# Kernel tuning notes

Hardware: AMD Instinct MI355X
Metric: run time of the kernel (lower is better)

The kernel has to match this reference:

```python
import jax, jax.numpy as jnp
import numpy as np

N_LOW, N_HIGH = 5000, 50000
E_LH, E_HH = 200000, 400000


def _gatv2(xs, xd, src, dst, Wl, bl, Wr, br, att, bias, n_dst):
    """PyG GATv2Conv with aggr='mean', concat heads. att: [H, C]."""
    H, C = att.shape
    hl = (xs @ Wl + bl).reshape(-1, H, C)   # source transform (messages)
    hr = (xd @ Wr + br).reshape(-1, H, C)   # target transform
    z = jax.nn.leaky_relu(hl[src] + hr[dst], 0.2)        # [E, H, C]
    logit = jnp.einsum('ehc,hc->eh', z, att)             # [E, H]
    m = jax.lax.stop_gradient(jax.ops.segment_max(logit, dst, num_segments=n_dst))
    ex = jnp.exp(logit - m[dst])
    s = jax.ops.segment_sum(ex, dst, num_segments=n_dst)
    alpha = ex / (s[dst] + 1e-16)                        # edge softmax per dst, per head
    msg = hl[src] * alpha[..., None]                     # [E, H, C]
    out = jax.ops.segment_sum(msg, dst, num_segments=n_dst)
    cnt = jax.ops.segment_sum(jnp.ones(dst.shape, xs.dtype), dst, num_segments=n_dst)
    out = out / jnp.maximum(cnt, 1.0)[:, None, None]     # aggr='mean'
    return out.reshape(n_dst, H * C) + bias


def _bn(x, g, b):
    mu = x.mean(0)
    var = x.var(0)
    return (x - mu) * jax.lax.rsqrt(var + 1e-5) * g + b


def setup_inputs() -> dict:
    key = jax.random.key(0)
    it = iter(jax.random.split(key, 64))
    def nk():
        return next(it)
    def glorot(shape):
        s = np.sqrt(2.0 / (shape[0] + shape[-1])).astype(np.float32)
        return jax.random.normal(nk(), shape, jnp.float32) * s
    inp = {}
    inp['xl'] = jax.random.normal(nk(), (N_LOW, 125), jnp.float32)
    inp['xh'] = jax.random.normal(nk(), (N_HIGH, 1), jnp.float32)
    inp['zstd'] = jax.random.normal(nk(), (N_HIGH, 1), jnp.float32)
    inp['si_lh'] = jax.random.randint(nk(), (E_LH,), 0, N_LOW, jnp.int32)
    inp['di_lh'] = jax.random.randint(nk(), (E_LH,), 0, N_HIGH, jnp.int32)
    inp['si_hh'] = jax.random.randint(nk(), (E_HH,), 0, N_HIGH, jnp.int32)
    inp['di_hh'] = jax.random.randint(nk(), (E_HH,), 0, N_HIGH, jnp.int32)
    def gat(pfx, fs, fd, H, C):
        inp[pfx + '_Wl'] = glorot((fs, H * C)); inp[pfx + '_bl'] = jnp.zeros((H * C,), jnp.float32)
        inp[pfx + '_Wr'] = glorot((fd, H * C)); inp[pfx + '_br'] = jnp.zeros((H * C,), jnp.float32)
        inp[pfx + '_att'] = glorot((H, C)); inp[pfx + '_b'] = jnp.zeros((H * C,), jnp.float32)
    gat('d', 125, 1, 1, 256)
    gat('p1', 257, 257, 4, 64)
    gat('p2', 256, 256, 4, 64)
    gat('p3', 256, 256, 1, 64)
    for pfx, dim in [('bn0', 257), ('bn1', 256), ('bn2', 256), ('bn3', 64)]:
        inp[pfx + '_g'] = jnp.ones((dim,), jnp.float32)
        inp[pfx + '_b'] = jnp.zeros((dim,), jnp.float32)
    inp['pr_W1'] = glorot((64, 64)); inp['pr_b1'] = jnp.zeros((64,), jnp.float32)
    inp['pr_W2'] = glorot((64, 1)); inp['pr_b2'] = jnp.zeros((1,), jnp.float32)
    return inp


def reference(xl, xh, zstd, si_lh, di_lh, si_hh, di_hh,
              d_Wl, d_bl, d_Wr, d_br, d_att, d_b,
              p1_Wl, p1_bl, p1_Wr, p1_br, p1_att, p1_b,
              p2_Wl, p2_bl, p2_Wr, p2_br, p2_att, p2_b,
              p3_Wl, p3_bl, p3_Wr, p3_br, p3_att, p3_b,
              bn0_g, bn0_b, bn1_g, bn1_b, bn2_g, bn2_b, bn3_g, bn3_b,
              pr_W1, pr_b1, pr_W2, pr_b2):
    n_high = xh.shape[0]
    # downscaler: bipartite GATv2 (low -> high), heads=1, no self loops
    enc = _gatv2(xl, xh, si_lh, di_lh, d_Wl, d_bl, d_Wr, d_br, d_att, d_b, n_high)
    x = jnp.concatenate([zstd, enc], axis=-1)            # [N_HIGH, 257]
    # high-within-high edges with self loops (add_self_loops=True)
    loop = jnp.arange(n_high, dtype=si_hh.dtype)
    src = jnp.concatenate([si_hh, loop])
    dst = jnp.concatenate([di_hh, loop])
    x = _bn(x, bn0_g, bn0_b)
    x = _gatv2(x, x, src, dst, p1_Wl, p1_bl, p1_Wr, p1_br, p1_att, p1_b, n_high)
    x = jax.nn.relu(_bn(x, bn1_g, bn1_b))
    x = _gatv2(x, x, src, dst, p2_Wl, p2_bl, p2_Wr, p2_br, p2_att, p2_b, n_high)
    x = jax.nn.relu(_bn(x, bn2_g, bn2_b))
    x = _gatv2(x, x, src, dst, p3_Wl, p3_bl, p3_Wr, p3_br, p3_att, p3_b, n_high)
    x = jax.nn.relu(_bn(x, bn3_g, bn3_b))
    # predictor MLP
    y = jax.nn.relu(x @ pr_W1 + pr_b1) @ pr_W2 + pr_b2   # [N_HIGH, 1]
    return y
```

## Files before the change

kernel.cpp:

```cpp
#include <hip/hip_runtime.h>
#include <math.h>

#define DEV __device__ __forceinline__

static const int N_LOW = 5000, N_HIGH = 50000, E_LH = 200000, E_HH = 400000;
static const int E2 = E_HH + N_HIGH;
static const int ETOT = E_LH + E2;
static const int RBLK = 2048;

typedef __attribute__((ext_vector_type(8))) short bf16x8;
typedef __attribute__((ext_vector_type(4))) float f32x4;
typedef __attribute__((ext_vector_type(8))) unsigned short u16x8;
typedef unsigned short u16;

DEV short f2bf(float v) {
    unsigned u = __float_as_uint(v);
    u += 0x7FFFu + ((u >> 16) & 1u);
    return (short)(u >> 16);
}
DEV float bf2f(u16 u) { return __uint_as_float(((unsigned)u) << 16); }

template <int VPL> struct RawTT { using T = u16; };
template <> struct RawTT<4> { using T = ushort4; };

template <bool RELU, bool BF16OUT>
DEV void gemm_body(const bf16x8* __restrict__ Af, const bf16x8* __restrict__ Bf,
                   const float* __restrict__ bias, float* __restrict__ C,
                   int M, int N, int nkt) {
    const int l = threadIdx.x & 63;
    const int w = threadIdx.x >> 6;
    const int nt0 = blockIdx.x * 4;
    const int mt0 = blockIdx.y * 8 + w * 2;
    f32x4 acc[2][4];
#pragma unroll
    for (int i = 0; i < 2; i++)
#pragma unroll
        for (int j = 0; j < 4; j++) acc[i][j] = (f32x4){0.f, 0.f, 0.f, 0.f};
    const bf16x8* a0p = Af + (size_t)mt0 * nkt * 64 + l;
    const bf16x8* a1p = a0p + (size_t)nkt * 64;
    const bf16x8* bp = Bf + (size_t)nt0 * nkt * 64 + l;
    for (int kt = 0; kt < nkt; kt++) {
        bf16x8 a0 = a0p[kt * 64];
        bf16x8 a1 = a1p[kt * 64];
        bf16x8 b0 = bp[kt * 64];
        bf16x8 b1 = bp[(size_t)(nkt + kt) * 64];
        bf16x8 b2 = bp[(size_t)(2 * nkt + kt) * 64];
        bf16x8 b3 = bp[(size_t)(3 * nkt + kt) * 64];
        acc[0][0] = __builtin_amdgcn_mfma_f32_16x16x32_bf16(a0, b0, acc[0][0], 0, 0, 0);
        acc[0][1] = __builtin_amdgcn_mfma_f32_16x16x32_bf16(a0, b1, acc[0][1], 0, 0, 0);
        acc[0][2] = __builtin_amdgcn_mfma_f32_16x16x32_bf16(a0, b2, acc[0][2], 0, 0, 0);
        acc[0][3] = __builtin_amdgcn_mfma_f32_16x16x32_bf16(a0, b3, acc[0][3], 0, 0, 0);
        acc[1][0] = __builtin_amdgcn_mfma_f32_16x16x32_bf16(a1, b0, acc[1][0], 0, 0, 0);
        acc[1][1] = __builtin_amdgcn_mfma_f32_16x16x32_bf16(a1, b1, acc[1][1], 0, 0, 0);
        acc[1][2] = __builtin_amdgcn_mfma_f32_16x16x32_bf16(a1, b2, acc[1][2], 0, 0, 0);
        acc[1][3] = __builtin_amdgcn_mfma_f32_16x16x32_bf16(a1, b3, acc[1][3], 0, 0, 0);
    }
    const int colb = nt0 * 16 + (l & 15);
    const int rsub = (l >> 4) * 4;
#pragma unroll
    for (int mi = 0; mi < 2; mi++) {
        int rowb = (mt0 + mi) * 16 + rsub;
#pragma unroll
        for (int r = 0; r < 4; r++) {
            int row = rowb + r;
            if (row >= M) continue;
#pragma unroll
            for (int n = 0; n < 4; n++) {
                int col = colb + n * 16;
                float v = acc[mi][n][r] + bias[col];
                if (RELU) v = fmaxf(v, 0.f);
                if (BF16OUT)
                    ((u16*)C)[(size_t)row * N + col] = (u16)f2bf(v);
                else
                    C[(size_t)row * N + col] = v;
            }
        }
    }
}

template <bool RELU, bool BF16OUT>
__global__ __launch_bounds__(256) void gemm_mfma(
    const bf16x8* __restrict__ Af, const bf16x8* __restrict__ Bf,
    const float* __restrict__ bias, float* __restrict__ C,
    int M, int N, int nkt) {
    gemm_body<RELU, BF16OUT>(Af, Bf, bias, C, M, N, nkt);
}

__global__ __launch_bounds__(256) void gemm_mfma2(
    const bf16x8* __restrict__ Af,
    const bf16x8* __restrict__ Bf0, const bf16x8* __restrict__ Bf1,
    const float* __restrict__ bias0, const float* __restrict__ bias1,
    float* __restrict__ C0, float* __restrict__ C1,
    int M, int N, int nkt) {
    if (blockIdx.z == 0)
        gemm_body<false, true>(Af, Bf0, bias0, C0, M, N, nkt);
    else
        gemm_body<false, true>(Af, Bf1, bias1, C1, M, N, nkt);
}

template <bool RELU>
__global__ __launch_bounds__(256) void bn_frag(
    const u16* __restrict__ x, int Nrows, int F, int STR, int SS,
    const float* __restrict__ sums,
    const float* __restrict__ g, const float* __restrict__ b,
    bf16x8* __restrict__ Af, int nmt, int nkt) {
    int total = nmt * nkt * 64;
    for (int idx = blockIdx.x * blockDim.x + threadIdx.x; idx < total;
         idx += gridDim.x * blockDim.x) {
        int mt = idx / (nkt * 64);
        int rem = idx - mt * (nkt * 64);
        int kt = rem >> 6, l = rem & 63;
        int row = mt * 16 + (l & 15);
        int colb = kt * 32 + (l >> 4) * 8;
        bf16x8 o;
#pragma unroll
        for (int j = 0; j < 8; j++) {
            int col = colb + j;
            float v = 0.f;
            if (row < Nrows && col < F) {
                float mu = sums[col] / Nrows;
                float var = sums[SS + col] / Nrows - mu * mu;
                float istd = rsqrtf(fmaxf(var, 0.f) + 1e-5f);
                v = (bf2f(x[(size_t)row * STR + col]) - mu) * istd * g[col] + b[col];
                if (RELU) v = fmaxf(v, 0.f);
            }
            o[j] = f2bf(v);
        }
        Af[idx] = o;
    }
}

__global__ __launch_bounds__(256) void cast_frag(
    const float* __restrict__ x, int Nrows, int F,
    bf16x8* __restrict__ Af, int nmt, int nkt) {
    int total = nmt * nkt * 64;
    for (int idx = blockIdx.x * blockDim.x + threadIdx.x; idx < total;
         idx += gridDim.x * blockDim.x) {
        int mt = idx / (nkt * 64);
        int rem = idx - mt * (nkt * 64);
        int kt = rem >> 6, l = rem & 63;
        int row = mt * 16 + (l & 15);
        int colb = kt * 32 + (l >> 4) * 8;
        bf16x8 o;
#pragma unroll
        for (int j = 0; j < 8; j++) {
            int col = colb + j;
            o[j] = (row < Nrows && col < F) ? f2bf(x[(size_t)row * F + col]) : (short)0;
        }
        Af[idx] = o;
    }
}

struct WtJobs {
    const float* W[8];
    bf16x8* out[8];
    int K[8], Nn[8], nnt[8], nkt[8];
};
__global__ __launch_bounds__(256) void wt_frag_all(WtJobs jobs) {
    const int job = blockIdx.y;
    const float* W = jobs.W[job];
    bf16x8* Bf = jobs.out[job];
    const int K = jobs.K[job], N = jobs.Nn[job];
    const int nkt = jobs.nkt[job];
    int total = jobs.nnt[job] * nkt * 64;
    for (int idx = blockIdx.x * blockDim.x + threadIdx.x; idx < total;
         idx += gridDim.x * blockDim.x) {
        int nt = idx / (nkt * 64);
        int rem = idx - nt * (nkt * 64);
        int kt = rem >> 6, l = rem & 63;
        int col = nt * 16 + (l & 15);
        int kb = kt * 32 + (l >> 4) * 8;
        bf16x8 o;
#pragma unroll
        for (int j = 0; j < 8; j++) {
            int k = kb + j;
            o[j] = (k < K && col < N) ? f2bf(W[(size_t)k * N + col]) : (short)0;
        }
        Bf[idx] = o;
    }
}

__global__ __launch_bounds__(256) void hist_all(
    const int* __restrict__ di_lh, const int* __restrict__ di_hh,
    int* __restrict__ cnt) {
    for (int i = blockIdx.x * blockDim.x + threadIdx.x; i < ETOT;
         i += gridDim.x * blockDim.x) {
        if (i < E_LH) {
            atomicAdd(&cnt[di_lh[i]], 1);
        } else {
            int j = i - E_LH;
            int d = (j < E_HH) ? di_hh[j] : (j - E_HH);
            atomicAdd(&cnt[N_HIGH + d], 1);
        }
    }
}

__global__ __launch_bounds__(256) void scan_partial(
    const int* __restrict__ cnt, int* __restrict__ off,
    int* __restrict__ bsum, int n) {
    __shared__ int s[256];
    const int t = threadIdx.x;
    const int base = blockIdx.x * 1024 + t * 4;
    int v0 = (base < n) ? cnt[base] : 0;
    int v1 = (base + 1 < n) ? cnt[base + 1] : 0;
    int v2 = (base + 2 < n) ? cnt[base + 2] : 0;
    int v3 = (base + 3 < n) ? cnt[base + 3] : 0;
    int tsum = v0 + v1 + v2 + v3;
    s[t] = tsum;
    __syncthreads();
    for (int step = 1; step < 256; step <<= 1) {
        int q = (t >= step) ? s[t - step] : 0;
        __syncthreads();
        s[t] += q;
        __syncthreads();
    }
    int excl = s[t] - tsum;
    if (base < n) off[base] = excl;
    if (base + 1 < n) off[base + 1] = excl + v0;
    if (base + 2 < n) off[base + 2] = excl + v0 + v1;
    if (base + 3 < n) off[base + 3] = excl + v0 + v1 + v2;
    if (t == 255) bsum[blockIdx.x] = s[255];
}

__global__ __launch_bounds__(256) void scan_bsums(
    int* __restrict__ bsum, int nb, int* __restrict__ off, int n) {
    __shared__ int s[256];
    const int t = threadIdx.x;
    int v = (t < nb) ? bsum[t] : 0;
    s[t] = v;
    __syncthreads();
    for (int step = 1; step < 256; step <<= 1) {
        int q = (t >= step) ? s[t - step] : 0;
        __syncthreads();
        s[t] += q;
        __syncthreads();
    }
    if (t < nb) bsum[t] = s[t] - v;
    if (t == 255) off[n] = s[255];
}

__global__ __launch_bounds__(256) void scan_add(
    int* __restrict__ off, const int* __restrict__ bsum, int n) {
    int b = blockIdx.x;
    int add = bsum[b];
    int base = b * 1024;
    int end = base + 1024 < n ? base + 1024 : n;
    for (int i = base + threadIdx.x; i < end; i += 256) off[i] += add;
}

__global__ __launch_bounds__(256) void scatter_all(
    const int* __restrict__ si_lh, const int* __restrict__ di_lh,
    const int* __restrict__ si_hh, const int* __restrict__ di_hh,
    int* __restrict__ cur, int* __restrict__ csr) {
    for (int i = blockIdx.x * blockDim.x + threadIdx.x; i < ETOT;
         i += gridDim.x * blockDim.x) {
        int d, s, bucket;
        if (i < E_LH) {
            d = di_lh[i]; s = si_lh[i]; bucket = d;
        } else {
            int j = i - E_LH;
            if (j < E_HH) { d = di_hh[j]; s = si_hh[j]; }
            else { d = s = j - E_HH; }
            bucket = N_HIGH + d;
        }
        int p = atomicAdd(&cur[bucket], 1);
        csr[p] = s;
    }
}

template <int H, int C, bool HR_ONFLY>
__global__ __launch_bounds__(256) void gat_gather(
    const u16* __restrict__ hl, const u16* __restrict__ hr,
    const float* __restrict__ xh, const float* __restrict__ Wr,
    const float* __restrict__ br,
    const int* __restrict__ rowptr, const int* __restrict__ csr_src,
    const float* __restrict__ att, const float* __restrict__ bias,
    u16* __restrict__ out, int outStride, int outOfs, int Ndst,
    const float* __restrict__ col0) {
    constexpr int HC = H * C;
    constexpr int VPL = HC / 64;
    constexpr int LPH = C / VPL;
    using RawT = typename RawTT<VPL>::T;
    int w = blockIdx.x * (blockDim.x >> 6) + (threadIdx.x >> 6);
    if (w >= Ndst) return;
    const int l = threadIdx.x & 63;

    float hrv[VPL], attv[VPL];
    if constexpr (HR_ONFLY) {
        static_assert(!HR_ONFLY || VPL == 4, "onfly assumes VPL==4");
        float xv = xh[w];
        float4 wr = *reinterpret_cast<const float4*>(Wr + l * 4);
        float4 bb = *reinterpret_cast<const float4*>(br + l * 4);
        hrv[0] = fmaf(xv, wr.x, bb.x); hrv[1] = fmaf(xv, wr.y, bb.y);
        hrv[2] = fmaf(xv, wr.z, bb.z); hrv[3] = fmaf(xv, wr.w, bb.w);
        float4 u = *reinterpret_cast<const float4*>(att + l * 4);
        attv[0] = u.x; attv[1] = u.y; attv[2] = u.z; attv[3] = u.w;
    } else if constexpr (VPL == 4) {
        ushort4 t = *(reinterpret_cast<const ushort4*>(hr + (size_t)w * HC) + l);
        hrv[0] = bf2f(t.x); hrv[1] = bf2f(t.y); hrv[2] = bf2f(t.z); hrv[3] = bf2f(t.w);
        float4 u = *reinterpret_cast<const float4*>(att + l * 4);
        attv[0] = u.x; attv[1] = u.y; attv[2] = u.z; attv[3] = u.w;
    } else {
#pragma unroll
        for (int j = 0; j < VPL; j++) {
            hrv[j] = bf2f(hr[(size_t)w * HC + l * VPL + j]);
            attv[j] = att[l * VPL + j];
        }
    }

    const int e0 = rowptr[w], e1 = rowptr[w + 1];
    float m = -3.4e38f, s = 0.f;
    float acc[VPL] = {};

    auto ldraw = [&](int sv) -> RawT {
        if constexpr (VPL == 4)
            return *(reinterpret_cast<const ushort4*>(hl + (size_t)sv * HC) + l);
        else
            return hl[(size_t)sv * HC + l];
    };
    auto proc = [&](RawT t) {
        float hlv[VPL];
        if constexpr (VPL == 4) {
            hlv[0] = bf2f(t.x); hlv[1] = bf2f(t.y);
            hlv[2] = bf2f(t.z); hlv[3] = bf2f(t.w);
        } else {
            hlv[0] = bf2f(t);
        }
        float v = 0.f;
#pragma unroll
        for (int j = 0; j < VPL; j++) {
            float z = hlv[j] + hrv[j];
            v = fmaf(fmaxf(z, 0.2f * z), attv[j], v);
        }
#pragma unroll
        for (int t2 = 1; t2 < LPH; t2 <<= 1) v += __shfl_xor(v, t2, 64);
        float d = v - m;
        bool up = d > 0.f;
        float ef = __expf(-fabsf(d));
        float sc = up ? ef : 1.f;
        float p  = up ? 1.f : ef;
        m = up ? v : m;
        s = fmaf(s, sc, p);
#pragma unroll
        for (int j = 0; j < VPL; j++) acc[j] = fmaf(acc[j], sc, p * hlv[j]);
    };

    int e = e0;
    for (; e + 3 < e1; e += 4) {
        int sv0 = csr_src[e];
        int sv1 = csr_src[e + 1];
        int sv2 = csr_src[e + 2];
        int sv3 = csr_src[e + 3];
        RawT t0 = ldraw(sv0);
        RawT t1 = ldraw(sv1);
        RawT t2 = ldraw(sv2);
        RawT t3 = ldraw(sv3);
        proc(t0); proc(t1); proc(t2); proc(t3);
    }
    for (; e < e1; e++) {
        RawT t = ldraw(csr_src[e]);
        proc(t);
    }

    float inv = 1.f / (s + 1e-16f);
    float dnorm = inv / fmaxf((float)(e1 - e0), 1.f);
    if constexpr (VPL == 4) {
        if (((outOfs | outStride) & 3) == 0) {
            ushort4 o;
            o.x = (u16)f2bf(acc[0] * dnorm + bias[l * 4 + 0]);
            o.y = (u16)f2bf(acc[1] * dnorm + bias[l * 4 + 1]);
            o.z = (u16)f2bf(acc[2] * dnorm + bias[l * 4 + 2]);
            o.w = (u16)f2bf(acc[3] * dnorm + bias[l * 4 + 3]);
            *(reinterpret_cast<ushort4*>(out + (size_t)w * outStride + outOfs) + l) = o;
        } else {
#pragma unroll
            for (int j = 0; j < 4; j++)
                out[(size_t)w * outStride + outOfs + l * 4 + j] =
                    (u16)f2bf(acc[j] * dnorm + bias[l * 4 + j]);
        }
    } else {
#pragma unroll
        for (int j = 0; j < VPL; j++)
            out[(size_t)w * outStride + outOfs + l * VPL + j] =
                (u16)f2bf(acc[j] * dnorm + bias[l * VPL + j]);
    }
    if (col0 && l == 0) out[(size_t)w * outStride] = (u16)f2bf(col0[w]);
}

template <int NC, int RPB>
__global__ __launch_bounds__(256) void bn_partial3(
    const u16* __restrict__ x, int Nrows, float* __restrict__ partials) {
    constexpr int STR = NC * 8;
    constexpr int NSTAT = 2 * NC * 8;
    const int t = threadIdx.x;
    const int b = blockIdx.x;
    __shared__ float l1[NC * RPB * 8];
    __shared__ float l2[NC * RPB * 8];
    float s1[8] = {}, s2[8] = {};
    if (t < NC * RPB) {
        const int rg = t / NC, cg = t - (t / NC) * NC;
        for (int r = b * RPB + rg; r < Nrows; r += RBLK * RPB) {
            u16x8 p = *reinterpret_cast<const u16x8*>(x + (size_t)r * STR + cg * 8);
#pragma unroll
            for (int j = 0; j < 8; j++) {
                float v = bf2f(p[j]);
                s1[j] += v; s2[j] += v * v;
            }
        }
#pragma unroll
        for (int j = 0; j < 8; j++) {
            l1[t * 8 + j] = s1[j];
            l2[t * 8 + j] = s2[j];
        }
    }
    __syncthreads();
    if (t < NC) {
        float a[8] = {}, c[8] = {};
#pragma unroll
        for (int rg = 0; rg < RPB; rg++)
#pragma unroll
            for (int j = 0; j < 8; j++) {
                a[j] += l1[(rg * NC + t) * 8 + j];
                c[j] += l2[(rg * NC + t) * 8 + j];
            }
#pragma unroll
        for (int j = 0; j < 8; j++) {
            partials[(size_t)b * NSTAT + t * 8 + j] = a[j];
            partials[(size_t)b * NSTAT + NC * 8 + t * 8 + j] = c[j];
        }
    }
}

__global__ __launch_bounds__(256) void bn_reduce2(
    const float* __restrict__ partials, int nstat, float* __restrict__ bsum) {
    const int sl = threadIdx.x & 63, ch = threadIdx.x >> 6;
    const int s = blockIdx.x * 64 + sl;
    const int b0 = blockIdx.y * (RBLK / 32);
    float v = 0.f;
    if (s < nstat) {
        for (int b = b0 + ch; b < b0 + RBLK / 32; b += 4)
            v += partials[(size_t)b * nstat + s];
    }
    __shared__ float l[256];
    l[threadIdx.x] = v;
    __syncthreads();
    if (ch == 0 && s < nstat)
        atomicAdd(&bsum[s], l[sl] + l[sl + 64] + l[sl + 128] + l[sl + 192]);
}

__global__ __launch_bounds__(256) void dot_w2(const float* __restrict__ hid,
                                              const float* __restrict__ W2,
                                              const float* __restrict__ b2,
                                              float* __restrict__ y, int N) {
    int w = blockIdx.x * (blockDim.x >> 6) + (threadIdx.x >> 6);
    int l = threadIdx.x & 63;
    if (w >= N) return;
    float v = hid[(size_t)w * 64 + l] * W2[l];
#pragma unroll
    for (int m = 1; m < 64; m <<= 1) v += __shfl_xor(v, m, 64);
    if (l == 0) y[w] = v + b2[0];
}

extern "C" void kernel_launch(void* const* d_in, const int* in_sizes, int n_in,
                              void* d_out, int out_size, void* d_ws, size_t ws_size,
                              hipStream_t stream) {
    const float* xl   = (const float*)d_in[0];
    const float* xh   = (const float*)d_in[1];
    const float* zstd = (const float*)d_in[2];
    const int* si_lh  = (const int*)d_in[3];
    const int* di_lh  = (const int*)d_in[4];
    const int* si_hh  = (const int*)d_in[5];
    const int* di_hh  = (const int*)d_in[6];
    int a = 7;
    const float *d_Wl = (const float*)d_in[a++], *d_bl = (const float*)d_in[a++],
                *d_Wr = (const float*)d_in[a++], *d_br = (const float*)d_in[a++],
                *d_att = (const float*)d_in[a++], *d_b = (const float*)d_in[a++];
    const float *p1_Wl = (const float*)d_in[a++], *p1_bl = (const float*)d_in[a++],
                *p1_Wr = (const float*)d_in[a++], *p1_br = (const float*)d_in[a++],
                *p1_att = (const float*)d_in[a++], *p1_b = (const float*)d_in[a++];
    const float *p2_Wl = (const float*)d_in[a++], *p2_bl = (const float*)d_in[a++],
                *p2_Wr = (const float*)d_in[a++], *p2_br = (const float*)d_in[a++],
                *p2_att = (const float*)d_in[a++], *p2_b = (const float*)d_in[a++];
    const float *p3_Wl = (const float*)d_in[a++], *p3_bl = (const float*)d_in[a++],
                *p3_Wr = (const float*)d_in[a++], *p3_br = (const float*)d_in[a++],
                *p3_att = (const float*)d_in[a++], *p3_b = (const float*)d_in[a++];
    const float *bn0_g = (const float*)d_in[a++], *bn0_b = (const float*)d_in[a++],
                *bn1_g = (const float*)d_in[a++], *bn1_b = (const float*)d_in[a++],
                *bn2_g = (const float*)d_in[a++], *bn2_b = (const float*)d_in[a++],
                *bn3_g = (const float*)d_in[a++], *bn3_b = (const float*)d_in[a++];
    const float *pr_W1 = (const float*)d_in[a++], *pr_b1 = (const float*)d_in[a++],
                *pr_W2 = (const float*)d_in[a++], *pr_b2 = (const float*)d_in[a++];
    float* y = (float*)d_out;

    const int N = N_HIGH;
    const int NMT = 3125;
    const int NB2 = (2 * N + 1023) / 1024;
    float* ws = (float*)d_ws;
    float* xA = ws;
    float* xB = xA + (size_t)N * 257;
    float* hl = xB + (size_t)N * 256;
    float* hr = hl + (size_t)N * 256;
    bf16x8* xl_f = (bf16x8*)(hr + (size_t)N * 256);
    bf16x8* wf_d   = xl_f + 320 * 4 * 64;
    bf16x8* wf_p1l = wf_d + 16 * 4 * 64;
    bf16x8* wf_p1r = wf_p1l + 16 * 9 * 64;
    bf16x8* wf_p2l = wf_p1r + 16 * 9 * 64;
    bf16x8* wf_p2r = wf_p2l + 16 * 8 * 64;
    bf16x8* wf_p3l = wf_p2r + 16 * 8 * 64;
    bf16x8* wf_p3r = wf_p3l + 4 * 8 * 64;
    bf16x8* wf_pr1 = wf_p3r + 4 * 8 * 64;
    float* bsum = (float*)(wf_pr1 + 4 * 2 * 64);
    int* bscan  = (int*)(bsum + 544);
    int* cnt    = bscan + 256;
    int* off    = cnt + 2 * N;
    int* cur    = off + 2 * N + 1;
    int* csr    = cur + 2 * N;
    size_t need = (size_t)((char*)(csr + ETOT) - (char*)ws);
    if (ws_size < need) return;
    bf16x8* AfB = (bf16x8*)xB;
    bf16x8* AfA = (bf16x8*)xA;
    u16* xA16 = (u16*)xA;
    u16* xB16 = (u16*)xB;
    u16* hl16 = (u16*)hl;
    u16* hr16 = (u16*)hr;
    float* partials = hr;
    int* rp_lh = off;
    int* rp_hh = off + N;

    dim3 blk(256);
    auto wgrid = [](int E) { return dim3((E + 3) / 4); };
    auto egrid = [](size_t total) {
        size_t g = (total + 255) / 256;
        return dim3((unsigned)(g > 2048 ? 2048 : g));
    };

    WtJobs jobs;
    jobs.W[0] = d_Wl;  jobs.out[0] = wf_d;   jobs.K[0] = 125; jobs.Nn[0] = 256; jobs.nnt[0] = 16; jobs.nkt[0] = 4;
    jobs.W[1] = p1_Wl; jobs.out[1] = wf_p1l; jobs.K[1] = 257; jobs.Nn[1] = 256; jobs.nnt[1] = 16; jobs.nkt[1] = 9;
    jobs.W[2] = p1_Wr; jobs.out[2] = wf_p1r; jobs.K[2] = 257; jobs.Nn[2] = 256; jobs.nnt[2] = 16; jobs.nkt[2] = 9;
    jobs.W[3] = p2_Wl; jobs.out[3] = wf_p2l; jobs.K[3] = 256; jobs.Nn[3] = 256; jobs.nnt[3] = 16; jobs.nkt[3] = 8;
    jobs.W[4] = p2_Wr; jobs.out[4] = wf_p2r; jobs.K[4] = 256; jobs.Nn[4] = 256; jobs.nnt[4] = 16; jobs.nkt[4] = 8;
    jobs.W[5] = p3_Wl; jobs.out[5] = wf_p3l; jobs.K[5] = 256; jobs.Nn[5] = 64;  jobs.nnt[5] = 4;  jobs.nkt[5] = 8;
    jobs.W[6] = p3_Wr; jobs.out[6] = wf_p3r; jobs.K[6] = 256; jobs.Nn[6] = 64;  jobs.nnt[6] = 4;  jobs.nkt[6] = 8;
    jobs.W[7] = pr_W1; jobs.out[7] = wf_pr1; jobs.K[7] = 64;  jobs.Nn[7] = 64;  jobs.nnt[7] = 4;  jobs.nkt[7] = 2;
    wt_frag_all<<<dim3(36, 8), blk, 0, stream>>>(jobs);
    cast_frag<<<dim3(320), blk, 0, stream>>>(xl, N_LOW, 125, xl_f, 320, 4);

    hipMemsetAsync(cnt, 0, 2 * (size_t)N * sizeof(int), stream);
    hist_all<<<egrid(ETOT), blk, 0, stream>>>(di_lh, di_hh, cnt);
    scan_partial<<<dim3(NB2), blk, 0, stream>>>(cnt, off, bscan, 2 * N);
    scan_bsums<<<dim3(1), blk, 0, stream>>>(bscan, NB2, off, 2 * N);
    scan_add<<<dim3(NB2), blk, 0, stream>>>(off, bscan, 2 * N);
    hipMemcpyAsync(cur, off, 2 * (size_t)N * sizeof(int), hipMemcpyDeviceToDevice, stream);
    scatter_all<<<egrid(ETOT), blk, 0, stream>>>(si_lh, di_lh, si_hh, di_hh, cur, csr);

    gemm_mfma<false, true><<<dim3(4, 40), blk, 0, stream>>>(xl_f, wf_d, d_bl, hl, N_LOW, 256, 4);
    gat_gather<1, 256, true><<<wgrid(N), blk, 0, stream>>>(
        hl16, nullptr, xh, d_Wr, d_br, rp_lh, csr, d_att, d_b, xA16, 264, 1, N, zstd);

    hipMemsetAsync(bsum, 0, 528 * sizeof(float), stream);
    bn_partial3<33, 7><<<dim3(RBLK), blk, 0, stream>>>(xA16, N, partials);
    bn_reduce2<<<dim3(9, 32), blk, 0, stream>>>(partials, 528, bsum);
    bn_frag<false><<<dim3(2048), blk, 0, stream>>>(xA16, N, 257, 264, 264, bsum, bn0_g, bn0_b, AfB, NMT, 9);

    gemm_mfma2<<<dim3(4, 391, 2), blk, 0, stream>>>(AfB, wf_p1l, wf_p1r, p1_bl, p1_br, hl, hr, N, 256, 9);
    gat_gather<4, 64, false><<<wgrid(N), blk, 0, stream>>>(
        hl16, hr16, nullptr, nullptr, nullptr, rp_hh, csr, p1_att, p1_b, xB16, 256, 0, N, nullptr);
    hipMemsetAsync(bsum, 0, 512 * sizeof(float), stream);
    bn_partial3<32, 8><<<dim3(RBLK), blk, 0, stream>>>(xB16, N, partials);
    bn_reduce2<<<dim3(8, 32), blk, 0, stream>>>(partials, 512, bsum);
    bn_frag<true><<<dim3(2048), blk, 0, stream>>>(xB16, N, 256, 256, 256, bsum, bn1_g, bn1_b, AfA, NMT, 8);

    gemm_mfma2<<<dim3(4, 391, 2), blk, 0, stream>>>(AfA, wf_p2l, wf_p2r, p2_bl, p2_br, hl, hr, N, 256, 8);
    gat_gather<4, 64, false><<<wgrid(N), blk, 0, stream>>>(
        hl16, hr16, nullptr, nullptr, nullptr, rp_hh, csr, p2_att, p2_b, xA16, 256, 0, N, nullptr);
    hipMemsetAsync(bsum, 0, 512 * sizeof(float), stream);
    bn_partial3<32, 8><<<dim3(RBLK), blk, 0, stream>>>(xA16, N, partials);
    bn_reduce2<<<dim3(8, 32), blk, 0, stream>>>(partials, 512, bsum);
    bn_frag<true><<<dim3(2048), blk, 0, stream>>>(xA16, N, 256, 256, 256, bsum, bn2_g, bn2_b, AfB, NMT, 8);

    gemm_mfma2<<<dim3(1, 391, 2), blk, 0, stream>>>(AfB, wf_p3l, wf_p3r, p3_bl, p3_br, hl, hr, N, 64, 8);
    gat_gather<1, 64, false><<<wgrid(N), blk, 0, stream>>>(
        hl16, hr16, nullptr, nullptr, nullptr, rp_hh, csr, p3_att, p3_b, xB16, 64, 0, N, nullptr);
    hipMemsetAsync(bsum, 0, 128 * sizeof(float), stream);
    bn_partial3<8, 32><<<dim3(RBLK), blk, 0, stream>>>(xB16, N, partials);
    bn_reduce2<<<dim3(2, 32), blk, 0, stream>>>(partials, 128, bsum);
    bn_frag<true><<<dim3(2048), blk, 0, stream>>>(xB16, N, 64, 64, 64, bsum, bn3_g, bn3_b, AfA, NMT, 2);

    gemm_mfma<true, false><<<dim3(1, 391), blk, 0, stream>>>(AfA, wf_pr1, pr_b1, hl, N, 64, 2);
    dot_w2<<<wgrid(N), blk, 0, stream>>>(hl, pr_W2, pr_b2, y, N);
}
```

Measured before the change: 531.1 us.

## Decompose leaky-relu attention logits into precomputed linear terms plus abs term

Uses leaky_relu(z)=0.6z+0.4|z| to split each edge logit into per-node dot products att·hl and att·hr, computed in the GEMM epilogue, plus an |z|·att term computed per edge. The gather kernel reads one extra float per edge instead of doing the full linear part there. It also replaces the branchy online softmax with a lazy-rescale variant that only updates the running max when the logit exceeds it by more than 8. This trades extra epilogue work, atomics for the downscaler layer and extra scalar loads for fewer per-edge ops. The lazy max may risk exp overflow or precision issues within the threshold.

```diff
diff --git a/kernel.cpp b/kernel.cpp
--- a/kernel.cpp
+++ b/kernel.cpp
@@ -23,10 +23,12 @@
 template <int VPL> struct RawTT { using T = u16; };
 template <> struct RawTT<4> { using T = ushort4; };
 
-template <bool RELU, bool BF16OUT>
+template <bool RELU, bool BF16OUT, int DOTM>
 DEV void gemm_body(const bf16x8* __restrict__ Af, const bf16x8* __restrict__ Bf,
                    const float* __restrict__ bias, float* __restrict__ C,
-                   int M, int N, int nkt) {
+                   int M, int N, int nkt,
+                   const float* __restrict__ att, float* __restrict__ dout,
+                   int Hh) {
     const int l = threadIdx.x & 63;
     const int w = threadIdx.x >> 6;
     const int nt0 = blockIdx.x * 4;
@@ -57,6 +59,16 @@
     }
     const int colb = nt0 * 16 + (l & 15);
     const int rsub = (l >> 4) * 4;
+    float attc[4];
+    float ds[2][4];
+    if constexpr (DOTM != 0) {
+#pragma unroll
+        for (int n = 0; n < 4; n++) attc[n] = att[colb + n * 16];
+#pragma unroll
+        for (int i = 0; i < 2; i++)
+#pragma unroll
+            for (int j = 0; j < 4; j++) ds[i][j] = 0.f;
+    }
 #pragma unroll
     for (int mi = 0; mi < 2; mi++) {
         int rowb = (mt0 + mi) * 16 + rsub;
@@ -69,21 +81,52 @@
                 int col = colb + n * 16;
                 float v = acc[mi][n][r] + bias[col];
                 if (RELU) v = fmaxf(v, 0.f);
-                if (BF16OUT)
-                    ((u16*)C)[(size_t)row * N + col] = (u16)f2bf(v);
-                else
+                if (BF16OUT) {
+                    u16 q = (u16)f2bf(v);
+                    ((u16*)C)[(size_t)row * N + col] = q;
+                    if constexpr (DOTM != 0)
+                        ds[mi][r] = fmaf(bf2f(q), attc[n], ds[mi][r]);
+                } else {
                     C[(size_t)row * N + col] = v;
+                }
             }
         }
     }
-}
-
-template <bool RELU, bool BF16OUT>
-__global__ __launch_bounds__(256) void gemm_mfma(
+    if constexpr (DOTM != 0) {
+#pragma unroll
+        for (int mi = 0; mi < 2; mi++) {
+#pragma unroll
+            for (int r = 0; r < 4; r++) {
+                float dsv = ds[mi][r];
+                dsv += __shfl_xor(dsv, 1, 64);
+                dsv += __shfl_xor(dsv, 2, 64);
+                dsv += __shfl_xor(dsv, 4, 64);
+                dsv += __shfl_xor(dsv, 8, 64);
+                int row = (mt0 + mi) * 16 + rsub + r;
+                if ((l & 15) == 0 && row < M) {
+                    if (DOTM == 1)
+                        dout[(size_t)row * Hh + blockIdx.x] = dsv;
+                    else
+                        atomicAdd(&dout[row], dsv);
+                }
+            }
+        }
+    }
+}
+
+__global__ __launch_bounds__(256) void gemm_plain(
     const bf16x8* __restrict__ Af, const bf16x8* __restrict__ Bf,
     const float* __restrict__ bias, float* __restrict__ C,
     int M, int N, int nkt) {
-    gemm_body<RELU, BF16OUT>(Af, Bf, bias, C, M, N, nkt);
+    gemm_body<true, false, 0>(Af, Bf, bias, C, M, N, nkt, nullptr, nullptr, 0);
+}
+
+__global__ __launch_bounds__(256) void gemm_dlayer(
+    const bf16x8* __restrict__ Af, const bf16x8* __restrict__ Bf,
+    const float* __restrict__ bias, float* __restrict__ C,
+    int M, int N, int nkt, const float* __restrict__ att,
+    float* __restrict__ dout) {
+    gemm_body<false, true, 2>(Af, Bf, bias, C, M, N, nkt, att, dout, 1);
 }
 
 __global__ __launch_bounds__(256) void gemm_mfma2(
@@ -91,11 +134,12 @@
     const bf16x8* __restrict__ Bf0, const bf16x8* __restrict__ Bf1,
     const float* __restrict__ bias0, const float* __restrict__ bias1,
     float* __restrict__ C0, float* __restrict__ C1,
-    int M, int N, int nkt) {
+    int M, int N, int nkt, const float* __restrict__ att,
+    float* __restrict__ dl, float* __restrict__ dr, int Hh) {
     if (blockIdx.z == 0)
-        gemm_body<false, true>(Af, Bf0, bias0, C0, M, N, nkt);
+        gemm_body<false, true, 1>(Af, Bf0, bias0, C0, M, N, nkt, att, dl, Hh);
     else
-        gemm_body<false, true>(Af, Bf1, bias1, C1, M, N, nkt);
+        gemm_body<false, true, 1>(Af, Bf1, bias1, C1, M, N, nkt, att, dr, Hh);
 }
 
 template <bool RELU>
@@ -273,6 +317,7 @@
     const u16* __restrict__ hl, const u16* __restrict__ hr,
     const float* __restrict__ xh, const float* __restrict__ Wr,
     const float* __restrict__ br,
+    const float* __restrict__ dl, const float* __restrict__ drt,
     const int* __restrict__ rowptr, const int* __restrict__ csr_src,
     const float* __restrict__ att, const float* __restrict__ bias,
     u16* __restrict__ out, int outStride, int outOfs, int Ndst,
@@ -284,8 +329,10 @@
     int w = blockIdx.x * (blockDim.x >> 6) + (threadIdx.x >> 6);
     if (w >= Ndst) return;
     const int l = threadIdx.x & 63;
+    const int h = (l * VPL) / C;
 
     float hrv[VPL], attv[VPL];
+    float drv;
     if constexpr (HR_ONFLY) {
         static_assert(!HR_ONFLY || VPL == 4, "onfly assumes VPL==4");
         float xv = xh[w];
@@ -295,17 +342,25 @@
         hrv[2] = fmaf(xv, wr.z, bb.z); hrv[3] = fmaf(xv, wr.w, bb.w);
         float4 u = *reinterpret_cast<const float4*>(att + l * 4);
         attv[0] = u.x; attv[1] = u.y; attv[2] = u.z; attv[3] = u.w;
+        float p = 0.f;
+#pragma unroll
+        for (int j = 0; j < 4; j++) p = fmaf(hrv[j], attv[j], p);
+#pragma unroll
+        for (int t2 = 1; t2 < LPH; t2 <<= 1) p += __shfl_xor(p, t2, 64);
+        drv = p;
     } else if constexpr (VPL == 4) {
         ushort4 t = *(reinterpret_cast<const ushort4*>(hr + (size_t)w * HC) + l);
         hrv[0] = bf2f(t.x); hrv[1] = bf2f(t.y); hrv[2] = bf2f(t.z); hrv[3] = bf2f(t.w);
         float4 u = *reinterpret_cast<const float4*>(att + l * 4);
         attv[0] = u.x; attv[1] = u.y; attv[2] = u.z; attv[3] = u.w;
+        drv = drt[(size_t)w * H + h];
     } else {
 #pragma unroll
         for (int j = 0; j < VPL; j++) {
             hrv[j] = bf2f(hr[(size_t)w * HC + l * VPL + j]);
             attv[j] = att[l * VPL + j];
         }
+        drv = drt[(size_t)w * H + h];
     }
 
     const int e0 = rowptr[w], e1 = rowptr[w + 1];
@@ -318,7 +373,7 @@
         else
             return hl[(size_t)sv * HC + l];
     };
-    auto proc = [&](RawT t) {
+    auto proc = [&](RawT t, float dlv) {
         float hlv[VPL];
         if constexpr (VPL == 4) {
             hlv[0] = bf2f(t.x); hlv[1] = bf2f(t.y);
@@ -326,23 +381,32 @@
         } else {
             hlv[0] = bf2f(t);
         }
-        float v = 0.f;
+        float red = 0.f;
 #pragma unroll
         for (int j = 0; j < VPL; j++) {
             float z = hlv[j] + hrv[j];
-            v = fmaf(fmaxf(z, 0.2f * z), attv[j], v);
-        }
-#pragma unroll
-        for (int t2 = 1; t2 < LPH; t2 <<= 1) v += __shfl_xor(v, t2, 64);
-        float d = v - m;
-        bool up = d > 0.f;
-        float ef = __expf(-fabsf(d));
-        float sc = up ? ef : 1.f;
-        float p  = up ? 1.f : ef;
-        m = up ? v : m;
-        s = fmaf(s, sc, p);
-#pragma unroll
-        for (int j = 0; j < VPL; j++) acc[j] = fmaf(acc[j], sc, p * hlv[j]);
+            red = fmaf(fabsf(z), attv[j], red);
+        }
+#pragma unroll
+        for (int t2 = 1; t2 < LPH; t2 <<= 1) red += __shfl_xor(red, t2, 64);
+        float v = fmaf(0.4f, red, 0.6f * (dlv + drv));
+        float dd = v - m;
+        if (__any(dd > 8.f)) {
+            bool up = dd > 8.f;
+            float arg = up ? -dd : dd;
+            float ef = __expf(arg);
+            float sc = up ? ef : 1.f;
+            float p  = up ? 1.f : ef;
+            m = up ? v : m;
+            s = fmaf(s, sc, p);
+#pragma unroll
+            for (int j = 0; j < VPL; j++) acc[j] = fmaf(acc[j], sc, p * hlv[j]);
+        } else {
+            float p = __expf(dd);
+            s += p;
+#pragma unroll
+            for (int j = 0; j < VPL; j++) acc[j] = fmaf(p, hlv[j], acc[j]);
+        }
     };
 
     int e = e0;
@@ -355,11 +419,17 @@
         RawT t1 = ldraw(sv1);
         RawT t2 = ldraw(sv2);
         RawT t3 = ldraw(sv3);
-        proc(t0); proc(t1); proc(t2); proc(t3);
+        float d0 = dl[(size_t)sv0 * H + h];
+        float d1 = dl[(size_t)sv1 * H + h];
+        float d2 = dl[(size_t)sv2 * H + h];
+        float d3 = dl[(size_t)sv3 * H + h];
+        proc(t0, d0); proc(t1, d1); proc(t2, d2); proc(t3, d3);
     }
     for (; e < e1; e++) {
-        RawT t = ldraw(csr_src[e]);
-        proc(t);
+        int sv = csr_src[e];
+        RawT t = ldraw(sv);
+        float dv = dl[(size_t)sv * H + h];
+        proc(t, dv);
     }
 
     float inv = 1.f / (s + 1e-16f);
@@ -515,7 +585,10 @@
     int* off    = cnt + 2 * N;
     int* cur    = off + 2 * N + 1;
     int* csr    = cur + 2 * N;
-    size_t need = (size_t)((char*)(csr + ETOT) - (char*)ws);
+    float* dl   = (float*)(csr + ETOT);
+    float* dr   = dl + 200000;
+    float* dl_d = dr + 200000;
+    size_t need = (size_t)((char*)(dl_d + N_LOW) - (char*)ws);
     if (ws_size < need) return;
     bf16x8* AfB = (bf16x8*)xB;
     bf16x8* AfA = (bf16x8*)xA;
@@ -554,39 +627,44 @@
     hipMemcpyAsync(cur, off, 2 * (size_t)N * sizeof(int), hipMemcpyDeviceToDevice, stream);
     scatter_all<<<egrid(ETOT), blk, 0, stream>>>(si_lh, di_lh, si_hh, di_hh, cur, csr);
 
-    gemm_mfma<false, true><<<dim3(4, 40), blk, 0, stream>>>(xl_f, wf_d, d_bl, hl, N_LOW, 256, 4);
+    hipMemsetAsync(dl_d, 0, (size_t)N_LOW * sizeof(float), stream);
+    gemm_dlayer<<<dim3(4, 40), blk, 0, stream>>>(xl_f, wf_d, d_bl, hl, N_LOW, 256, 4, d_att, dl_d);
     gat_gather<1, 256, true><<<wgrid(N), blk, 0, stream>>>(
-        hl16, nullptr, xh, d_Wr, d_br, rp_lh, csr, d_att, d_b, xA16, 264, 1, N, zstd);
+        hl16, nullptr, xh, d_Wr, d_br, dl_d, nullptr, rp_lh, csr, d_att, d_b,
+        xA16, 264, 1, N, zstd);
 
     hipMemsetAsync(bsum, 0, 528 * sizeof(float), stream);
     bn_partial3<33, 7><<<dim3(RBLK), blk, 0, stream>>>(xA16, N, partials);
     bn_reduce2<<<dim3(9, 32), blk, 0, stream>>>(partials, 528, bsum);
     bn_frag<false><<<dim3(2048), blk, 0, stream>>>(xA16, N, 257, 264, 264, bsum, bn0_g, bn0_b, AfB, NMT, 9);
 
-    gemm_mfma2<<<dim3(4, 391, 2), blk, 0, stream>>>(AfB, wf_p1l, wf_p1r, p1_bl, p1_br, hl, hr, N, 256, 9);
+    gemm_mfma2<<<dim3(4, 391, 2), blk, 0, stream>>>(AfB, wf_p1l, wf_p1r, p1_bl, p1_br, hl, hr, N, 256, 9, p1_att, dl, dr, 4);
     gat_gather<4, 64, false><<<wgrid(N), blk, 0, stream>>>(
-        hl16, hr16, nullptr, nullptr, nullptr, rp_hh, csr, p1_att, p1_b, xB16, 256, 0, N, nullptr);
+        hl16, hr16, nullptr, nullptr, nullptr, dl, dr, rp_hh, csr, p1_att, p1_b,
+        xB16, 256, 0, N, nullptr);
     hipMemsetAsync(bsum, 0, 512 * sizeof(float), stream);
     bn_partial3<32, 8><<<dim3(RBLK), blk, 0, stream>>>(xB16, N, partials);
     bn_reduce2<<<dim3(8, 32), blk, 0, stream>>>(partials, 512, bsum);
     bn_frag<true><<<dim3(2048), blk, 0, stream>>>(xB16, N, 256, 256, 256, bsum, bn1_g, bn1_b, AfA, NMT, 8);
 
-    gemm_mfma2<<<dim3(4, 391, 2), blk, 0, stream>>>(AfA, wf_p2l, wf_p2r, p2_bl, p2_br, hl, hr, N, 256, 8);
+    gemm_mfma2<<<dim3(4, 391, 2), blk, 0, stream>>>(AfA, wf_p2l, wf_p2r, p2_bl, p2_br, hl, hr, N, 256, 8, p2_att, dl, dr, 4);
     gat_gather<4, 64, false><<<wgrid(N), blk, 0, stream>>>(
-        hl16, hr16, nullptr, nullptr, nullptr, rp_hh, csr, p2_att, p2_b, xA16, 256, 0, N, nullptr);
+        hl16, hr16, nullptr, nullptr, nullptr, dl, dr, rp_hh, csr, p2_att, p2_b,
+        xA16, 256, 0, N, nullptr);
     hipMemsetAsync(bsum, 0, 512 * sizeof(float), stream);
     bn_partial3<32, 8><<<dim3(RBLK), blk, 0, stream>>>(xA16, N, partials);
     bn_reduce2<<<dim3(8, 32), blk, 0, stream>>>(partials, 512, bsum);
     bn_frag<true><<<dim3(2048), blk, 0, stream>>>(xA16, N, 256, 256, 256, bsum, bn2_g, bn2_b, AfB, NMT, 8);
 
-    gemm_mfma2<<<dim3(1, 391, 2), blk, 0, stream>>>(AfB, wf_p3l, wf_p3r, p3_bl, p3_br, hl, hr, N, 64, 8);
+    gemm_mfma2<<<dim3(1, 391, 2), blk, 0, stream>>>(AfB, wf_p3l, wf_p3r, p3_bl, p3_br, hl, hr, N, 64, 8, p3_att, dl, dr, 1);
     gat_gather<1, 64, false><<<wgrid(N), blk, 0, stream>>>(
-        hl16, hr16, nullptr, nullptr, nullptr, rp_hh, csr, p3_att, p3_b, xB16, 64, 0, N, nullptr);
+        hl16, hr16, nullptr, nullptr, nullptr, dl, dr, rp_hh, csr, p3_att, p3_b,
+        xB16, 64, 0, N, nullptr);
     hipMemsetAsync(bsum, 0, 128 * sizeof(float), stream);
     bn_partial3<8, 32><<<dim3(RBLK), blk, 0, stream>>>(xB16, N, partials);
     bn_reduce2<<<dim3(2, 32), blk, 0, stream>>>(partials, 128, bsum);
     bn_frag<true><<<dim3(2048), blk, 0, stream>>>(xB16, N, 64, 64, 64, bsum, bn3_g, bn3_b, AfA, NMT, 2);
 
-    gemm_mfma<true, false><<<dim3(1, 391), blk, 0, stream>>>(AfA, wf_pr1, pr_b1, hl, N, 64, 2);
+    gemm_plain<<<dim3(1, 391), blk, 0, stream>>>(AfA, wf_pr1, pr_b1, hl, N, 64, 2);
     dot_w2<<<wgrid(N), blk, 0, stream>>>(hl, pr_W2, pr_b2, y, N);
 }
```

Measured after the change: 566.3 us. 1.07x slower.
